# Kernel optimization log

Hardware: AMD Instinct MI355X
Metric: run time of the kernel (lower is better)

Reference implementation:

```python
import jax, jax.numpy as jnp
import numpy as np

B, S, D, H = 4, 2048, 1024, 16
HD = D // H

def rotate_half(x):
    x1, x2 = jnp.split(x, 2, axis=-1)
    return jnp.concatenate((-x2, x1), axis=-1)

def apply_rope(x, cos, sin):
    # x: [B,H,S,hd]; cos/sin: [S,hd] -> broadcast over B,H
    return x * cos[None, None] + rotate_half(x) * sin[None, None]

def setup_inputs() -> dict:
    key = jax.random.key(0)
    ks = jax.random.split(key, 8)
    x = jax.random.normal(ks[0], (B, S, D), dtype=jnp.float32)
    mask = jnp.triu(jnp.ones((S, S), dtype=bool), k=1)  # True = masked (causal)
    pos = jnp.arange(S, dtype=jnp.float32)[:, None]
    inv = 1.0 / (10000.0 ** (jnp.arange(0, HD, 2, dtype=jnp.float32) / HD))
    ang = pos * inv[None, :]  # [S, hd/2]
    ang = jnp.concatenate([ang, ang], axis=-1)  # [S, hd]
    rope_cos = jnp.cos(ang)
    rope_sin = jnp.sin(ang)
    scale = 1.0 / np.sqrt(D)
    Wq = jax.random.normal(ks[1], (D, D), dtype=jnp.float32) * scale
    Wk = jax.random.normal(ks[2], (D, D), dtype=jnp.float32) * scale
    Wv = jax.random.normal(ks[3], (D, D), dtype=jnp.float32) * scale
    Wo = jax.random.normal(ks[4], (D, D), dtype=jnp.float32) * scale
    z = jnp.zeros((D,), dtype=jnp.float32)
    return {"x": x, "mask": mask, "rope_cos": rope_cos, "rope_sin": rope_sin,
            "Wq": Wq, "bq": z, "Wk": Wk, "bk": z, "Wv": Wv, "bv": z, "Wo": Wo, "bo": z}

def reference(x, mask, rope_cos, rope_sin, Wq, bq, Wk, bk, Wv, bv, Wo, bo):
    b, s, d = x.shape
    def proj(W, bias):
        y = x @ W.T + bias  # torch Linear: x W^T + b
        return y.reshape(b, s, H, HD).transpose(0, 2, 1, 3)  # [B,H,S,hd]
    Q = apply_rope(proj(Wq, bq), rope_cos, rope_sin)
    K = apply_rope(proj(Wk, bk), rope_cos, rope_sin)
    V = proj(Wv, bv)
    scores = jnp.einsum('bhqd,bhkd->bhqk', Q, K) / jnp.sqrt(jnp.float32(HD))
    scores = jnp.where(mask[None, None], -jnp.inf, scores)
    attn = jax.nn.softmax(scores, axis=-1)
    ctx = jnp.einsum('bhqk,bhkd->bhqd', attn, V)
    ctx = ctx.transpose(0, 2, 1, 3).reshape(b, s, d)
    return ctx @ Wo.T + bo
```

## Files before the change

### kernel.cpp

```cpp
#include <hip/hip_runtime.h>
#include <hip/hip_bf16.h>

#define S_LEN 2048
#define D_MODEL 1024
#define NH 16
#define HDIM 64
#define B_SZ 4

typedef __attribute__((ext_vector_type(8))) short bf16x8;
typedef __attribute__((ext_vector_type(4))) float f32x4;

__device__ inline void gld16(const __hip_bfloat16* g, __hip_bfloat16* l) {
    __builtin_amdgcn_global_load_lds(
        (const __attribute__((address_space(1))) unsigned int*)g,
        (__attribute__((address_space(3))) unsigned int*)l, 16, 0, 0);
}

__device__ inline unsigned int pkbf(float a, float b) {
    float2 f; f.x = a; f.y = b;
    __hip_bfloat162 h = __float22bfloat162_rn(f);
    union { __hip_bfloat162 h; unsigned int u; } cv; cv.h = h; return cv.u;
}

__global__ __launch_bounds__(256) void f2bf4_kernel(const float4* __restrict__ in,
                                                    __hip_bfloat162* __restrict__ out,
                                                    int n4) {
    int i = blockIdx.x * 256 + threadIdx.x;
    if (i < n4) {
        float4 v = in[i];
        __hip_bfloat162 a, b;
        a.x = __float2bfloat16(v.x); a.y = __float2bfloat16(v.y);
        b.x = __float2bfloat16(v.z); b.y = __float2bfloat16(v.w);
        out[2 * i]     = a;
        out[2 * i + 1] = b;
    }
}

__global__ __launch_bounds__(256) void f2bfw_kernel(
    const float4* __restrict__ w0, const float4* __restrict__ w1,
    const float4* __restrict__ w2, const float4* __restrict__ w3,
    __hip_bfloat162* __restrict__ o0, __hip_bfloat162* __restrict__ o1,
    __hip_bfloat162* __restrict__ o2, __hip_bfloat162* __restrict__ o3) {
    const int z = blockIdx.y;
    const float4* in = (z == 0) ? w0 : (z == 1) ? w1 : (z == 2) ? w2 : w3;
    __hip_bfloat162* out = (z == 0) ? o0 : (z == 1) ? o1 : (z == 2) ? o2 : o3;
    int i = blockIdx.x * 256 + threadIdx.x;
    float4 v = in[i];
    __hip_bfloat162 a, b;
    a.x = __float2bfloat16(v.x); a.y = __float2bfloat16(v.y);
    b.x = __float2bfloat16(v.z); b.y = __float2bfloat16(v.w);
    out[2 * i]     = a;
    out[2 * i + 1] = b;
}

__device__ inline void gemm_mainloop(const __hip_bfloat16* __restrict__ X,
                                     const __hip_bfloat16* __restrict__ W,
                                     __hip_bfloat16* As, __hip_bfloat16* Bs,
                                     int m0, int n0, f32x4 acc[4][4]) {
    const int tid = threadIdx.x;
    const int wv = tid >> 6, lane = tid & 63, l15 = lane & 15, quad = lane >> 4;
    const int rw = (wv >> 1) * 64, cw = (wv & 1) * 64;
    const int row_s = tid >> 3;
    const int csw = ((tid & 7) ^ (row_s & 7)) * 8;
    const __hip_bfloat16* xsrc = X + (size_t)(m0 + row_s) * D_MODEL + csw;
    const __hip_bfloat16* wsrc = W + (size_t)(n0 + row_s) * D_MODEL + csw;
    const int ld = tid * 8;

    auto stage = [&](int k0, int bsel) {
#pragma unroll
        for (int i = 0; i < 4; i++) {
            gld16(xsrc + (size_t)(i * 32) * D_MODEL + k0,
                  &As[bsel * 8192 + i * 2048 + ld]);
            gld16(wsrc + (size_t)(i * 32) * D_MODEL + k0,
                  &Bs[bsel * 8192 + i * 2048 + ld]);
        }
    };

    stage(0, 0);
    __syncthreads();
    for (int kt = 0; kt < 16; kt++) {
        const int buf = kt & 1;
        if (kt + 1 < 16) stage((kt + 1) * 64, buf ^ 1);
        const __hip_bfloat16* Ab = &As[buf * 8192];
        const __hip_bfloat16* Bb = &Bs[buf * 8192];
#pragma unroll
        for (int kc = 0; kc < 2; kc++) {
            bf16x8 af[4], bfr[4];
#pragma unroll
            for (int t = 0; t < 4; t++)
                af[t] = *(const bf16x8*)&Ab[(rw + t * 16 + l15) * 64 +
                                            (((kc * 4 + quad) ^ (l15 & 7)) * 8)];
#pragma unroll
            for (int t = 0; t < 4; t++)
                bfr[t] = *(const bf16x8*)&Bb[(cw + t * 16 + l15) * 64 +
                                             (((kc * 4 + quad) ^ (l15 & 7)) * 8)];
#pragma unroll
            for (int mt = 0; mt < 4; mt++)
#pragma unroll
                for (int nt = 0; nt < 4; nt++)
                    acc[mt][nt] = __builtin_amdgcn_mfma_f32_16x16x32_bf16(
                        af[mt], bfr[nt], acc[mt][nt], 0, 0, 0);
        }
        __syncthreads();
    }
}

#define PT 136
__global__ __launch_bounds__(256, 2) void qkv_kernel(
    const __hip_bfloat16* __restrict__ X,
    const __hip_bfloat16* __restrict__ W0, const __hip_bfloat16* __restrict__ W1,
    const __hip_bfloat16* __restrict__ W2,
    const float* __restrict__ b0, const float* __restrict__ b1,
    const float* __restrict__ b2,
    const float* __restrict__ rc, const float* __restrict__ rs,
    __hip_bfloat16* __restrict__ Qo, __hip_bfloat16* __restrict__ Ko,
    __hip_bfloat16* __restrict__ Vo) {
    __shared__ __hip_bfloat16 pool[32768];
    __hip_bfloat16* As = pool;
    __hip_bfloat16* Bs = pool + 16384;
    const int z = blockIdx.z;
    const __hip_bfloat16* W = (z == 0) ? W0 : ((z == 1) ? W1 : W2);
    const float* bias = (z == 0) ? b0 : ((z == 1) ? b1 : b2);
    f32x4 acc[4][4];
#pragma unroll
    for (int i = 0; i < 4; i++)
#pragma unroll
        for (int j = 0; j < 4; j++) acc[i][j] = (f32x4){0.f, 0.f, 0.f, 0.f};
    const int m0 = blockIdx.x * 128, n0 = blockIdx.y * 128;
    gemm_mainloop(X, W, As, Bs, m0, n0, acc);

    const int tid = threadIdx.x;
    const int wv = tid >> 6, lane = tid & 63, l15 = lane & 15, quad = lane >> 4;
    const int rw = (wv >> 1) * 64, cw = (wv & 1) * 64;

    if (z == 2) {
        __hip_bfloat16* T = pool;
        const int b = m0 >> 11, s0l = m0 & (S_LEN - 1);
#pragma unroll
        for (int hn = 0; hn < 2; hn++) {
            __syncthreads();
            if ((wv & 1) == hn) {
#pragma unroll
                for (int mt = 0; mt < 4; mt++)
#pragma unroll
                    for (int nt = 0; nt < 4; nt++)
#pragma unroll
                        for (int r = 0; r < 4; r++) {
                            int dl = nt * 16 + l15;
                            int ml = rw + mt * 16 + quad * 4 + r;
                            T[dl * PT + ml] =
                                __float2bfloat16(acc[mt][nt][r] + bias[n0 + hn * 64 + dl]);
                        }
            }
            __syncthreads();
            const int d = tid >> 2, sc = tid & 3;
            const int h = (n0 >> 6) + hn;
            size_t gb = ((size_t)((b * NH + h) * HDIM + d)) * S_LEN + s0l + sc * 32;
#pragma unroll
            for (int j = 0; j < 4; j++) {
                bf16x8 v = *(const bf16x8*)&T[d * PT + sc * 32 + j * 8];
                *(bf16x8*)&Vo[gb + j * 8] = v;
            }
        }
    } else {
        __hip_bfloat16* dst = (z == 0) ? Qo : Ko;
        const float qs = (z == 0) ? 0.18033688011112042f : 1.0f;
#pragma unroll
        for (int mt = 0; mt < 4; mt++)
#pragma unroll
            for (int r = 0; r < 4; r++) {
                int m = m0 + rw + mt * 16 + quad * 4 + r;
                int s = m & (S_LEN - 1), b = m >> 11;
#pragma unroll
                for (int nt = 0; nt < 2; nt++) {
                    int n1 = n0 + cw + nt * 16 + l15;
                    int h = n1 >> 6, hd1 = n1 & 63;
                    float y1 = acc[mt][nt][r] + bias[n1];
                    float y2 = acc[mt][nt + 2][r] + bias[n1 + 32];
                    float c1 = rc[s * HDIM + hd1], s1 = rs[s * HDIM + hd1];
                    float c2 = rc[s * HDIM + hd1 + 32], s2 = rs[s * HDIM + hd1 + 32];
                    size_t base = (((size_t)(b * NH + h)) * S_LEN + s) * HDIM;
                    dst[base + hd1]      = __float2bfloat16((y1 * c1 - y2 * s1) * qs);
                    dst[base + hd1 + 32] = __float2bfloat16((y2 * c2 + y1 * s2) * qs);
                }
            }
    }
}

#define SWZ(r, c) (((r) << 6) + ((c) ^ (((r) & 7) << 3)))
__global__ __launch_bounds__(256) void attn_kernel(
    const __hip_bfloat16* __restrict__ Q, const __hip_bfloat16* __restrict__ K,
    const __hip_bfloat16* __restrict__ VT, __hip_bfloat16* __restrict__ CTX) {
    __shared__ __hip_bfloat16 Kl[2][64 * 64];
    __shared__ __hip_bfloat16 Vl[2][64 * 64];
    __shared__ __hip_bfloat16 Pl[4][16 * 64];
    const int tid = threadIdx.x;
    const int wv = tid >> 6, lane = tid & 63, l15 = lane & 15, quad = lane >> 4;
    const int bh = blockIdx.x;
    const int pr = blockIdx.y;
    const int tA = pr, tC = 31 - pr;
    const int nkb = tC + 1;
    const size_t off = (size_t)bh * S_LEN * HDIM;
    const __hip_bfloat16* Qp = Q + off;
    const __hip_bfloat16* Kp = K + off;
    const __hip_bfloat16* Vp = VT + off;
    __hip_bfloat16* Pw = &Pl[wv][0];

    const int e0 = wv * 512 + lane * 8;
    const int r0 = e0 >> 6, c80 = e0 & 63;
    const int sw0 = c80 ^ ((r0 & 7) << 3);
    const int r1 = r0 + 32;
    const int sw1 = c80 ^ ((r1 & 7) << 3);
    const __hip_bfloat16* ks0 = Kp + r0 * 64 + sw0;
    const __hip_bfloat16* ks1 = Kp + r1 * 64 + sw1;
    const __hip_bfloat16* vs0 = Vp + (size_t)r0 * S_LEN + sw0;
    const __hip_bfloat16* vs1 = Vp + (size_t)r1 * S_LEN + sw1;

    auto stage = [&](int kb, int bsel) {
        const int ko = kb * 64;
        gld16(ks0 + (size_t)ko * 64, &Kl[bsel][e0]);
        gld16(ks1 + (size_t)ko * 64, &Kl[bsel][e0 + 2048]);
        gld16(vs0 + ko, &Vl[bsel][e0]);
        gld16(vs1 + ko, &Vl[bsel][e0 + 2048]);
    };

    bf16x8 qfA[2], qfC[2];
#pragma unroll
    for (int c = 0; c < 2; c++) {
        qfA[c] = *(const bf16x8*)&Qp[(size_t)(tA * 64 + wv * 16 + l15) * HDIM + c * 32 + quad * 8];
        qfC[c] = *(const bf16x8*)&Qp[(size_t)(tC * 64 + wv * 16 + l15) * HDIM + c * 32 + quad * 8];
    }

    float lA = 0.f, lC = 0.f;
    f32x4 accA[4], accC[4];
#pragma unroll
    for (int nt = 0; nt < 4; nt++) {
        accA[nt] = (f32x4){0.f, 0.f, 0.f, 0.f};
        accC[nt] = (f32x4){0.f, 0.f, 0.f, 0.f};
    }

    const int qrel = wv * 16 + l15;

    stage(0, 0);
    __syncthreads();
    for (int kb = 0; kb < nkb; kb++) {
        const int buf = kb & 1;
        if (kb + 1 < nkb) stage(kb + 1, buf ^ 1);
        const __hip_bfloat16* Kb_ = &Kl[buf][0];
        const __hip_bfloat16* Vb_ = &Vl[buf][0];

        const bool aAct = (kb <= tA);
        unsigned int pk[8];

        f32x4 saC[4], saA[4];
#pragma unroll
        for (int st = 0; st < 4; st++) {
            saC[st] = (f32x4){0.f, 0.f, 0.f, 0.f};
            saA[st] = (f32x4){0.f, 0.f, 0.f, 0.f};
        }
        if (aAct) {
#pragma unroll
            for (int c = 0; c < 2; c++)
#pragma unroll
                for (int st = 0; st < 4; st++) {
                    bf16x8 kf = *(const bf16x8*)&Kb_[SWZ(st * 16 + l15, c * 32 + quad * 8)];
                    saC[st] = __builtin_amdgcn_mfma_f32_16x16x32_bf16(kf, qfC[c], saC[st], 0, 0, 0);
                    saA[st] = __builtin_amdgcn_mfma_f32_16x16x32_bf16(kf, qfA[c], saA[st], 0, 0, 0);
                }
        } else {
#pragma unroll
            for (int c = 0; c < 2; c++)
#pragma unroll
                for (int st = 0; st < 4; st++) {
                    bf16x8 kf = *(const bf16x8*)&Kb_[SWZ(st * 16 + l15, c * 32 + quad * 8)];
                    saC[st] = __builtin_amdgcn_mfma_f32_16x16x32_bf16(kf, qfC[c], saC[st], 0, 0, 0);
                }
        }

        {
            float ls = 0.f;
            if (kb == tC) {
#pragma unroll
                for (int st = 0; st < 4; st++) {
                    float p[4];
#pragma unroll
                    for (int r = 0; r < 4; r++) {
                        bool msk = (st * 16 + quad * 4 + r > qrel);
                        p[r] = msk ? 0.f : __builtin_exp2f(saC[st][r]);
                        ls += p[r];
                    }
                    pk[st * 2 + 0] = pkbf(p[0], p[1]);
                    pk[st * 2 + 1] = pkbf(p[2], p[3]);
                }
            } else {
#pragma unroll
                for (int st = 0; st < 4; st++) {
                    float p[4];
#pragma unroll
                    for (int r = 0; r < 4; r++) {
                        p[r] = __builtin_exp2f(saC[st][r]);
                        ls += p[r];
                    }
                    pk[st * 2 + 0] = pkbf(p[0], p[1]);
                    pk[st * 2 + 1] = pkbf(p[2], p[3]);
                }
            }
            ls += __shfl_xor(ls, 16);
            ls += __shfl_xor(ls, 32);
            lC += ls;
#pragma unroll
            for (int st = 0; st < 4; st++) {
                uint2 w; w.x = pk[st * 2]; w.y = pk[st * 2 + 1];
                *(uint2*)&Pw[SWZ(l15, st * 16 + quad * 4)] = w;
            }
#pragma unroll
            for (int c = 0; c < 2; c++) {
                bf16x8 vf[4];
#pragma unroll
                for (int nt = 0; nt < 4; nt++)
                    vf[nt] = *(const bf16x8*)&Vb_[SWZ(nt * 16 + l15, c * 32 + quad * 8)];
                bf16x8 pf = *(const bf16x8*)&Pw[SWZ(l15, c * 32 + quad * 8)];
#pragma unroll
                for (int nt = 0; nt < 4; nt++)
                    accC[nt] = __builtin_amdgcn_mfma_f32_16x16x32_bf16(vf[nt], pf, accC[nt], 0, 0, 0);
            }
        }
        if (aAct) {
            float ls = 0.f;
            if (kb == tA) {
#pragma unroll
                for (int st = 0; st < 4; st++) {
                    float p[4];
#pragma unroll
                    for (int r = 0; r < 4; r++) {
                        bool msk = (st * 16 + quad * 4 + r > qrel);
                        p[r] = msk ? 0.f : __builtin_exp2f(saA[st][r]);
                        ls += p[r];
                    }
                    pk[st * 2 + 0] = pkbf(p[0], p[1]);
                    pk[st * 2 + 1] = pkbf(p[2], p[3]);
                }
            } else {
#pragma unroll
                for (int st = 0; st < 4; st++) {
                    float p[4];
#pragma unroll
                    for (int r = 0; r < 4; r++) {
                        p[r] = __builtin_exp2f(saA[st][r]);
                        ls += p[r];
                    }
                    pk[st * 2 + 0] = pkbf(p[0], p[1]);
                    pk[st * 2 + 1] = pkbf(p[2], p[3]);
                }
            }
            ls += __shfl_xor(ls, 16);
            ls += __shfl_xor(ls, 32);
            lA += ls;
#pragma unroll
            for (int st = 0; st < 4; st++) {
                uint2 w; w.x = pk[st * 2]; w.y = pk[st * 2 + 1];
                *(uint2*)&Pw[SWZ(l15, st * 16 + quad * 4)] = w;
            }
#pragma unroll
            for (int c = 0; c < 2; c++) {
                bf16x8 vf[4];
#pragma unroll
                for (int nt = 0; nt < 4; nt++)
                    vf[nt] = *(const bf16x8*)&Vb_[SWZ(nt * 16 + l15, c * 32 + quad * 8)];
                bf16x8 pf = *(const bf16x8*)&Pw[SWZ(l15, c * 32 + quad * 8)];
#pragma unroll
                for (int nt = 0; nt < 4; nt++)
                    accA[nt] = __builtin_amdgcn_mfma_f32_16x16x32_bf16(vf[nt], pf, accA[nt], 0, 0, 0);
            }
        }

        __syncthreads();
    }

    const int b = bh >> 4, h = bh & 15;
    {
        const int q = tA * 64 + wv * 16 + l15;
        const float inv = 1.0f / lA;
#pragma unroll
        for (int nt = 0; nt < 4; nt++) {
            uint2 st2;
            st2.x = pkbf(accA[nt][0] * inv, accA[nt][1] * inv);
            st2.y = pkbf(accA[nt][2] * inv, accA[nt][3] * inv);
            *(uint2*)&CTX[((size_t)(b * S_LEN + q)) * D_MODEL + h * HDIM + nt * 16 + quad * 4] = st2;
        }
    }
    {
        const int q = tC * 64 + wv * 16 + l15;
        const float inv = 1.0f / lC;
#pragma unroll
        for (int nt = 0; nt < 4; nt++) {
            uint2 st2;
            st2.x = pkbf(accC[nt][0] * inv, accC[nt][1] * inv);
            st2.y = pkbf(accC[nt][2] * inv, accC[nt][3] * inv);
            *(uint2*)&CTX[((size_t)(b * S_LEN + q)) * D_MODEL + h * HDIM + nt * 16 + quad * 4] = st2;
        }
    }
}

__global__ __launch_bounds__(256, 2) void outproj_kernel(
    const __hip_bfloat16* __restrict__ X, const __hip_bfloat16* __restrict__ W,
    const float* __restrict__ bias, float* __restrict__ OUT) {
    __shared__ __hip_bfloat16 As[2 * 8192];
    __shared__ __hip_bfloat16 Bs[2 * 8192];
    f32x4 acc[4][4];
#pragma unroll
    for (int i = 0; i < 4; i++)
#pragma unroll
        for (int j = 0; j < 4; j++) acc[i][j] = (f32x4){0.f, 0.f, 0.f, 0.f};
    const int m0 = blockIdx.x * 128, n0 = blockIdx.y * 128;
    gemm_mainloop(X, W, As, Bs, m0, n0, acc);
    const int tid = threadIdx.x;
    const int wv = tid >> 6, lane = tid & 63, l15 = lane & 15, quad = lane >> 4;
    const int rw = (wv >> 1) * 64, cw = (wv & 1) * 64;
#pragma unroll
    for (int mt = 0; mt < 4; mt++)
#pragma unroll
        for (int r = 0; r < 4; r++) {
            int m = m0 + rw + mt * 16 + quad * 4 + r;
#pragma unroll
            for (int nt = 0; nt < 4; nt++) {
                int n = n0 + cw + nt * 16 + l15;
                OUT[(size_t)m * D_MODEL + n] = acc[mt][nt][r] + bias[n];
            }
        }
}

extern "C" void kernel_launch(void* const* d_in, const int* in_sizes, int n_in,
                              void* d_out, int out_size, void* d_ws, size_t ws_size,
                              hipStream_t stream) {
    const float* x  = (const float*)d_in[0];
    const float* rc = (const float*)d_in[2];
    const float* rs = (const float*)d_in[3];
    const float* Wq = (const float*)d_in[4];
    const float* bq = (const float*)d_in[5];
    const float* Wk = (const float*)d_in[6];
    const float* bk = (const float*)d_in[7];
    const float* Wv = (const float*)d_in[8];
    const float* bv = (const float*)d_in[9];
    const float* Wo = (const float*)d_in[10];
    const float* bo = (const float*)d_in[11];

    char* ws = (char*)d_ws;
    __hip_bfloat16* xbf = (__hip_bfloat16*)(ws);
    __hip_bfloat16* wqb = (__hip_bfloat16*)(ws + (16u << 20));
    __hip_bfloat16* wkb = (__hip_bfloat16*)(ws + (18u << 20));
    __hip_bfloat16* wvb = (__hip_bfloat16*)(ws + (20u << 20));
    __hip_bfloat16* wob = (__hip_bfloat16*)(ws + (22u << 20));
    __hip_bfloat16* Qb  = (__hip_bfloat16*)(ws + (24u << 20));
    __hip_bfloat16* Kb  = (__hip_bfloat16*)(ws + (40u << 20));
    __hip_bfloat16* Vb  = (__hip_bfloat16*)(ws + (56u << 20));
    __hip_bfloat16* Cb  = (__hip_bfloat16*)(ws + (72u << 20));
    float* out = (float*)d_out;

    f2bf4_kernel<<<8192, 256, 0, stream>>>((const float4*)x, (__hip_bfloat162*)xbf, 2097152);
    f2bfw_kernel<<<dim3(1024, 4), 256, 0, stream>>>(
        (const float4*)Wq, (const float4*)Wk, (const float4*)Wv, (const float4*)Wo,
        (__hip_bfloat162*)wqb, (__hip_bfloat162*)wkb, (__hip_bfloat162*)wvb,
        (__hip_bfloat162*)wob);

    qkv_kernel<<<dim3(64, 8, 3), 256, 0, stream>>>(xbf, wqb, wkb, wvb, bq, bk, bv,
                                                   rc, rs, Qb, Kb, Vb);
    attn_kernel<<<dim3(64, 16), 256, 0, stream>>>(Qb, Kb, Vb, Cb);
    outproj_kernel<<<dim3(64, 8), 256, 0, stream>>>(Cb, wob, bo, out);
}
```

Before: 290.1 us.

## Load V fragments directly from global, merge conversion kernels, raise attention occupancy

```diff
diff --git a/kernel.cpp b/kernel.cpp
--- a/kernel.cpp
+++ b/kernel.cpp
@@ -22,29 +22,27 @@
     union { __hip_bfloat162 h; unsigned int u; } cv; cv.h = h; return cv.u;
 }
 
-__global__ __launch_bounds__(256) void f2bf4_kernel(const float4* __restrict__ in,
-                                                    __hip_bfloat162* __restrict__ out,
-                                                    int n4) {
-    int i = blockIdx.x * 256 + threadIdx.x;
-    if (i < n4) {
-        float4 v = in[i];
-        __hip_bfloat162 a, b;
-        a.x = __float2bfloat16(v.x); a.y = __float2bfloat16(v.y);
-        b.x = __float2bfloat16(v.z); b.y = __float2bfloat16(v.w);
-        out[2 * i]     = a;
-        out[2 * i + 1] = b;
-    }
-}
-
-__global__ __launch_bounds__(256) void f2bfw_kernel(
+__global__ __launch_bounds__(256) void conv_kernel(
+    const float4* __restrict__ x,
     const float4* __restrict__ w0, const float4* __restrict__ w1,
     const float4* __restrict__ w2, const float4* __restrict__ w3,
+    __hip_bfloat162* __restrict__ xo,
     __hip_bfloat162* __restrict__ o0, __hip_bfloat162* __restrict__ o1,
     __hip_bfloat162* __restrict__ o2, __hip_bfloat162* __restrict__ o3) {
-    const int z = blockIdx.y;
-    const float4* in = (z == 0) ? w0 : (z == 1) ? w1 : (z == 2) ? w2 : w3;
-    __hip_bfloat162* out = (z == 0) ? o0 : (z == 1) ? o1 : (z == 2) ? o2 : o3;
-    int i = blockIdx.x * 256 + threadIdx.x;
+    const int id = blockIdx.x;
+    const float4* in;
+    __hip_bfloat162* out;
+    int i;
+    if (id < 8192) {
+        in = x; out = xo;
+        i = id * 256 + threadIdx.x;
+    } else {
+        const int r = id - 8192;
+        const int z = r >> 10;
+        in  = (z == 0) ? w0 : (z == 1) ? w1 : (z == 2) ? w2 : w3;
+        out = (z == 0) ? o0 : (z == 1) ? o1 : (z == 2) ? o2 : o3;
+        i = (r & 1023) * 256 + threadIdx.x;
+    }
     float4 v = in[i];
     __hip_bfloat162 a, b;
     a.x = __float2bfloat16(v.x); a.y = __float2bfloat16(v.y);
@@ -188,11 +186,10 @@
 }
 
 #define SWZ(r, c) (((r) << 6) + ((c) ^ (((r) & 7) << 3)))
-__global__ __launch_bounds__(256) void attn_kernel(
+__global__ __launch_bounds__(256, 4) void attn_kernel(
     const __hip_bfloat16* __restrict__ Q, const __hip_bfloat16* __restrict__ K,
     const __hip_bfloat16* __restrict__ VT, __hip_bfloat16* __restrict__ CTX) {
     __shared__ __hip_bfloat16 Kl[2][64 * 64];
-    __shared__ __hip_bfloat16 Vl[2][64 * 64];
     __shared__ __hip_bfloat16 Pl[4][16 * 64];
     const int tid = threadIdx.x;
     const int wv = tid >> 6, lane = tid & 63, l15 = lane & 15, quad = lane >> 4;
@@ -213,15 +210,12 @@
     const int sw1 = c80 ^ ((r1 & 7) << 3);
     const __hip_bfloat16* ks0 = Kp + r0 * 64 + sw0;
     const __hip_bfloat16* ks1 = Kp + r1 * 64 + sw1;
-    const __hip_bfloat16* vs0 = Vp + (size_t)r0 * S_LEN + sw0;
-    const __hip_bfloat16* vs1 = Vp + (size_t)r1 * S_LEN + sw1;
+    const __hip_bfloat16* vbase = Vp + (size_t)l15 * S_LEN + quad * 8;
 
     auto stage = [&](int kb, int bsel) {
         const int ko = kb * 64;
         gld16(ks0 + (size_t)ko * 64, &Kl[bsel][e0]);
         gld16(ks1 + (size_t)ko * 64, &Kl[bsel][e0 + 2048]);
-        gld16(vs0 + ko, &Vl[bsel][e0]);
-        gld16(vs1 + ko, &Vl[bsel][e0 + 2048]);
     };
 
     bf16x8 qfA[2], qfC[2];
@@ -247,7 +241,6 @@
         const int buf = kb & 1;
         if (kb + 1 < nkb) stage(kb + 1, buf ^ 1);
         const __hip_bfloat16* Kb_ = &Kl[buf][0];
-        const __hip_bfloat16* Vb_ = &Vl[buf][0];
 
         const bool aAct = (kb <= tA);
         unsigned int pk[8];
@@ -275,6 +268,16 @@
                     bf16x8 kf = *(const bf16x8*)&Kb_[SWZ(st * 16 + l15, c * 32 + quad * 8)];
                     saC[st] = __builtin_amdgcn_mfma_f32_16x16x32_bf16(kf, qfC[c], saC[st], 0, 0, 0);
                 }
+        }
+
+        bf16x8 vf[2][4];
+        {
+            const __hip_bfloat16* vk = vbase + kb * 64;
+#pragma unroll
+            for (int c = 0; c < 2; c++)
+#pragma unroll
+                for (int nt = 0; nt < 4; nt++)
+                    vf[c][nt] = *(const bf16x8*)(vk + (size_t)(nt * 16) * S_LEN + c * 32);
         }
 
         {
@@ -315,14 +318,10 @@
             }
 #pragma unroll
             for (int c = 0; c < 2; c++) {
-                bf16x8 vf[4];
+                bf16x8 pf = *(const bf16x8*)&Pw[SWZ(l15, c * 32 + quad * 8)];
 #pragma unroll
                 for (int nt = 0; nt < 4; nt++)
-                    vf[nt] = *(const bf16x8*)&Vb_[SWZ(nt * 16 + l15, c * 32 + quad * 8)];
-                bf16x8 pf = *(const bf16x8*)&Pw[SWZ(l15, c * 32 + quad * 8)];
-#pragma unroll
-                for (int nt = 0; nt < 4; nt++)
-                    accC[nt] = __builtin_amdgcn_mfma_f32_16x16x32_bf16(vf[nt], pf, accC[nt], 0, 0, 0);
+                    accC[nt] = __builtin_amdgcn_mfma_f32_16x16x32_bf16(vf[c][nt], pf, accC[nt], 0, 0, 0);
             }
         }
         if (aAct) {
@@ -363,14 +362,10 @@
             }
 #pragma unroll
             for (int c = 0; c < 2; c++) {
-                bf16x8 vf[4];
+                bf16x8 pf = *(const bf16x8*)&Pw[SWZ(l15, c * 32 + quad * 8)];
 #pragma unroll
                 for (int nt = 0; nt < 4; nt++)
-                    vf[nt] = *(const bf16x8*)&Vb_[SWZ(nt * 16 + l15, c * 32 + quad * 8)];
-                bf16x8 pf = *(const bf16x8*)&Pw[SWZ(l15, c * 32 + quad * 8)];
-#pragma unroll
-                for (int nt = 0; nt < 4; nt++)
-                    accA[nt] = __builtin_amdgcn_mfma_f32_16x16x32_bf16(vf[nt], pf, accA[nt], 0, 0, 0);
+                    accA[nt] = __builtin_amdgcn_mfma_f32_16x16x32_bf16(vf[c][nt], pf, accA[nt], 0, 0, 0);
             }
         }
 
@@ -457,11 +452,11 @@
     __hip_bfloat16* Cb  = (__hip_bfloat16*)(ws + (72u << 20));
     float* out = (float*)d_out;
 
-    f2bf4_kernel<<<8192, 256, 0, stream>>>((const float4*)x, (__hip_bfloat162*)xbf, 2097152);
-    f2bfw_kernel<<<dim3(1024, 4), 256, 0, stream>>>(
-        (const float4*)Wq, (const float4*)Wk, (const float4*)Wv, (const float4*)Wo,
-        (__hip_bfloat162*)wqb, (__hip_bfloat162*)wkb, (__hip_bfloat162*)wvb,
-        (__hip_bfloat162*)wob);
+    conv_kernel<<<12288, 256, 0, stream>>>(
+        (const float4*)x, (const float4*)Wq, (const float4*)Wk,
+        (const float4*)Wv, (const float4*)Wo,
+        (__hip_bfloat162*)xbf, (__hip_bfloat162*)wqb, (__hip_bfloat162*)wkb,
+        (__hip_bfloat162*)wvb, (__hip_bfloat162*)wob);
 
     qkv_kernel<<<dim3(64, 8, 3), 256, 0, stream>>>(xbf, wqb, wkb, wvb, bq, bk, bv,
                                                    rc, rs, Qb, Kb, Vb);
```

Result: slower. 371.9 us (+28.2%).
